# Kernel optimization log

Measured on AMD Instinct MI355X. Metric: run time of the kernel, lower is better.

The kernel has to match this reference:

```python
import jax, jax.numpy as jnp
import numpy as np

B, T, C = 4, 2048, 1024
Q_DIM, KV_DIM, VOCAB = 256, 32, 50257
N_LAYER, LAYER_ID = 24, 12
SCORE_SCALE, CAP_SCALE = 1024.0, 64.0
EPS = 1e-5


def _init_shift_coef(dim, power):
    ratio = 1.0 - LAYER_ID / max(N_LAYER, 1)
    ddd = np.arange(dim, dtype=np.float32) / max(dim - 1, 1)
    return jnp.asarray(1.0 - np.power(ddd, power * ratio), dtype=jnp.float32).reshape(1, 1, dim)


def setup_inputs() -> dict:
    key = jax.random.key(0)
    ks = jax.random.split(key, 10)
    x = jax.random.normal(ks[0], (B, T, C), dtype=jnp.float32)
    idx = jax.random.randint(ks[1], (B, T), 0, VOCAB, dtype=jnp.int64)
    u = lambda k, shape, a: jax.random.uniform(k, shape, jnp.float32, -a, a)
    W_qq = u(ks[2], (Q_DIM, C), 0.5 / C ** 0.5)
    W_k = u(ks[3], (KV_DIM, C), 0.05 / C ** 0.5)
    W_kup = u(ks[4], (Q_DIM, KV_DIM), 0.05 / KV_DIM ** 0.5)
    W_v = u(ks[5], (KV_DIM, C), 0.05 / C ** 0.5)
    W_vup = u(ks[6], (C, KV_DIM), 0.05 / KV_DIM ** 0.5)
    k_emb_tab = 0.02 * jax.random.normal(ks[7], (VOCAB, Q_DIM), dtype=jnp.float32)
    v_emb_tab = 0.02 * jax.random.normal(ks[8], (VOCAB, C), dtype=jnp.float32)
    return dict(
        x=x, idx=idx,
        W_qq=W_qq, W_k=W_k, W_kup=W_kup, W_v=W_v, W_vup=W_vup,
        k_emb_tab=k_emb_tab, v_emb_tab=v_emb_tab,
        x_q=_init_shift_coef(Q_DIM, 0.2),
        x_k=_init_shift_coef(Q_DIM, 0.7),
        x_v=_init_shift_coef(C, 0.7),
        g_q=jnp.ones((Q_DIM,), jnp.float32), b_q=jnp.zeros((Q_DIM,), jnp.float32),
        g_k=jnp.ones((Q_DIM,), jnp.float32), b_k=jnp.zeros((Q_DIM,), jnp.float32),
        g_v=jnp.ones((C,), jnp.float32), b_v=jnp.zeros((C,), jnp.float32),
    )


def _time_shift(t):
    # ZeroPad2d((0,0,1,-1)): shift sequence right by one, zero at position 0
    return jnp.pad(t, ((0, 0), (1, 0), (0, 0)))[:, :-1, :]


def _layernorm(t, g, b):
    mu = jnp.mean(t, axis=-1, keepdims=True)
    var = jnp.var(t, axis=-1, keepdims=True)
    return (t - mu) * jax.lax.rsqrt(var + EPS) * g + b


def reference(x, idx, W_qq, W_k, W_kup, W_v, W_vup, k_emb_tab, v_emb_tab,
              x_q, x_k, x_v, g_q, b_q, g_k, b_k, g_v, b_v):
    k_emb = k_emb_tab[idx]            # [B,T,Q_DIM]
    v_emb = v_emb_tab[idx]            # [B,T,C]

    q = jnp.einsum('btc,qc->btq', x, W_qq)
    q = q + (_time_shift(q) - q) * x_q
    q = _layernorm(q, g_q, b_q)

    k = jnp.einsum('btd,qd->btq', jnp.einsum('btc,dc->btd', x, W_k), W_kup) * k_emb
    k = k + (_time_shift(k) - k) * x_k
    k = _layernorm(k, g_k, b_k)

    v = jnp.tanh(jnp.einsum('btd,cd->btc', jnp.einsum('btc,dc->btd', x, W_v), W_vup)) * v_emb
    v = v + (_time_shift(v) - v) * x_v
    v = _layernorm(v, g_v, b_v)

    scores = jnp.einsum('btq,bsq->bts', q, k) / SCORE_SCALE   # [B,T,T]
    scores = CAP_SCALE * jnp.tanh(scores)
    causal = jnp.tril(jnp.ones((T, T), dtype=bool))
    scores = jnp.where(causal[None], scores, -jnp.inf)
    attn = jax.nn.softmax(scores.astype(jnp.float32), axis=-1).astype(scores.dtype)
    out = jnp.einsum('bts,bsc->btc', attn, v)                 # [B,T,C]
    return out
```

## Files before the change

### kernel.cpp

```cpp
#include <hip/hip_runtime.h>

#define B_   4
#define T_   2048
#define C_   1024
#define QD   256
#define KVD  32
#define NR   (B_*T_)
#define EPSF 1e-5f
#define CAPS 64.0f
#define INV_SS (1.0f/1024.0f)
#define SPLITROWS 4608

typedef __attribute__((ext_vector_type(8))) short bf16x8;
typedef __attribute__((ext_vector_type(4))) short bf16x4;
typedef __attribute__((ext_vector_type(4))) float f32x4;

__device__ __forceinline__ float bf2f(unsigned short h) {
    return __uint_as_float(((unsigned)h) << 16);
}
__device__ __forceinline__ unsigned short f2bf(float f) {
    unsigned u = __float_as_uint(f);
    u = u + 0x7fffu + ((u >> 16) & 1u);
    return (unsigned short)(u >> 16);
}
__device__ __forceinline__ float ldf(const void* p, long i, int isbf) {
    return isbf ? bf2f(((const unsigned short*)p)[i]) : ((const float*)p)[i];
}
__device__ __forceinline__ long ldix(const void* p, long i, int is64) {
    return is64 ? (long)((const long long*)p)[i] : (long)((const int*)p)[i];
}
__device__ __forceinline__ float fast_tanh(float v) {
    float u = __expf(2.0f * v);
    return 1.0f - 2.0f / (u + 1.0f);
}

__global__ void detect_kernel(const void* x, const void* idxp, int* flags) {
    __shared__ int cnt[2];
    int tid = threadIdx.x;
    if (tid < 2) cnt[tid] = 0;
    __syncthreads();
    int pl = 0;
    const unsigned short* u = (const unsigned short*)x;
    for (int r = 0; r < 2; r++) {
        long j = 2L * (((long)(tid * 2 + r) * 15013L) % 4000000L);
        unsigned short v = u[j];
        int e = (v >> 7) & 0xff;
        pl += (v == 0 || (e >= 100 && e <= 140)) ? 1 : 0;
    }
    atomicAdd(&cnt[0], pl);
    const unsigned* w = (const unsigned*)idxp;
    int z = (w[2 * tid + 1] == 0u) ? 1 : 0;
    atomicAdd(&cnt[1], z);
    __syncthreads();
    if (tid == 0) {
        flags[0] = (cnt[0] > 384) ? 1 : 0;
        flags[1] = (cnt[1] > 128) ? 1 : 0;
    }
}

template<int BN, int TANH, int EMB>
__global__ __launch_bounds__(256) void gemm_kernel(
    const void* __restrict__ A, const void* __restrict__ W,
    const void* __restrict__ emb, const void* __restrict__ idxp,
    float* __restrict__ Cout, int M, int K, int N, int embN, int amode,
    const int* __restrict__ flags)
{
    const int fbf = flags[0];
    const int abf = amode ? fbf : 0;
    const int i64 = flags[1];

    __shared__ float As[32][68];
    __shared__ float Bs[32][BN + 4];

    const int tid = threadIdx.x;
    const long m0 = (long)blockIdx.x * 64;
    const int  n0 = blockIdx.y * BN;
    constexpr int TN = (BN == 64) ? 4 : 2;
    const int tx = tid & 15;
    const int ty = tid >> 4;

    float c[4][TN];
#pragma unroll
    for (int i = 0; i < 4; i++)
#pragma unroll
        for (int j = 0; j < TN; j++) c[i][j] = 0.0f;

    for (int k0 = 0; k0 < K; k0 += 32) {
        {
            int i = tid >> 2;
            int j0 = (tid & 3) * 8;
            long base = (m0 + i) * (long)K + k0 + j0;
            if (abf) {
                bf16x8 av = *reinterpret_cast<const bf16x8*>((const unsigned short*)A + base);
#pragma unroll
                for (int jj = 0; jj < 8; jj++) As[j0 + jj][i] = bf2f((unsigned short)av[jj]);
            } else {
                const float4* ap = reinterpret_cast<const float4*>((const float*)A + base);
                float4 f0 = ap[0], f1 = ap[1];
                As[j0 + 0][i] = f0.x; As[j0 + 1][i] = f0.y;
                As[j0 + 2][i] = f0.z; As[j0 + 3][i] = f0.w;
                As[j0 + 4][i] = f1.x; As[j0 + 5][i] = f1.y;
                As[j0 + 6][i] = f1.z; As[j0 + 7][i] = f1.w;
            }
        }
        if (BN == 64) {
            int n = tid >> 2;
            int j0 = (tid & 3) * 8;
            long base = (long)(n0 + n) * K + k0 + j0;
            if (fbf) {
                bf16x8 bv = *reinterpret_cast<const bf16x8*>((const unsigned short*)W + base);
#pragma unroll
                for (int jj = 0; jj < 8; jj++) Bs[j0 + jj][n] = bf2f((unsigned short)bv[jj]);
            } else {
                const float4* bp = reinterpret_cast<const float4*>((const float*)W + base);
                float4 f0 = bp[0], f1 = bp[1];
                Bs[j0 + 0][n] = f0.x; Bs[j0 + 1][n] = f0.y;
                Bs[j0 + 2][n] = f0.z; Bs[j0 + 3][n] = f0.w;
                Bs[j0 + 4][n] = f1.x; Bs[j0 + 5][n] = f1.y;
                Bs[j0 + 6][n] = f1.z; Bs[j0 + 7][n] = f1.w;
            }
        } else {
            int n = tid >> 3;
            int j0 = (tid & 7) * 4;
            long base = (long)(n0 + n) * K + k0 + j0;
            if (fbf) {
                bf16x4 bv = *reinterpret_cast<const bf16x4*>((const unsigned short*)W + base);
#pragma unroll
                for (int jj = 0; jj < 4; jj++) Bs[j0 + jj][n] = bf2f((unsigned short)bv[jj]);
            } else {
                float4 f0 = *reinterpret_cast<const float4*>((const float*)W + base);
                Bs[j0 + 0][n] = f0.x; Bs[j0 + 1][n] = f0.y;
                Bs[j0 + 2][n] = f0.z; Bs[j0 + 3][n] = f0.w;
            }
        }
        __syncthreads();
#pragma unroll
        for (int kk = 0; kk < 32; kk++) {
            const float4 af = *reinterpret_cast<const float4*>(&As[kk][ty * 4]);
            const float av[4] = {af.x, af.y, af.z, af.w};
            float bv[TN];
#pragma unroll
            for (int j = 0; j < TN; j++) bv[j] = Bs[kk][tx * TN + j];
#pragma unroll
            for (int i = 0; i < 4; i++)
#pragma unroll
                for (int j = 0; j < TN; j++) c[i][j] = fmaf(av[i], bv[j], c[i][j]);
        }
        __syncthreads();
    }

#pragma unroll
    for (int i = 0; i < 4; i++) {
        long row = m0 + ty * 4 + i;
        long id = 0;
        if (EMB) id = ldix(idxp, row, i64);
        float ev[TN];
        if (EMB && TN == 4) {
            long ebase = id * (long)embN + n0 + tx * 4;
            if (fbf) {
                bf16x4 e4 = *reinterpret_cast<const bf16x4*>((const unsigned short*)emb + ebase);
#pragma unroll
                for (int j = 0; j < 4; j++) ev[j] = bf2f((unsigned short)e4[j]);
            } else {
                float4 e4 = *reinterpret_cast<const float4*>((const float*)emb + ebase);
                ev[0] = e4.x; ev[1] = e4.y; ev[2] = e4.z; ev[3] = e4.w;
            }
        }
#pragma unroll
        for (int j = 0; j < TN; j++) {
            int col = n0 + tx * TN + j;
            float v = c[i][j];
            if (TANH) v = fast_tanh(v);
            if (EMB)  v *= (TN == 4) ? ev[j] : ldf(emb, id * (long)embN + col, fbf);
            Cout[row * (long)N + col] = v;
        }
    }
}

template<int DIM>
__global__ __launch_bounds__(256) void shiftln_kernel(
    const float* __restrict__ src, void* __restrict__ dst, int dst_bf16,
    const void* __restrict__ xs, const void* __restrict__ g,
    const void* __restrict__ bb, const int* __restrict__ flags)
{
    const int fbf = flags[0];
    const long r = blockIdx.x;
    const int t = (int)(r % T_);
    const int tid = threadIdx.x;
    constexpr int PT = DIM / 256;
    float m[PT];
    float s1 = 0.0f, s2 = 0.0f;
#pragma unroll
    for (int j = 0; j < PT; j++) {
        int o = tid + 256 * j;
        float v  = src[r * DIM + o];
        float pv = (t > 0) ? src[(r - 1) * DIM + o] : 0.0f;
        float xv = ldf(xs, o, fbf);
        float mm = v + (pv - v) * xv;
        m[j] = mm;
        s1 += mm;
        s2 += mm * mm;
    }
#pragma unroll
    for (int off = 32; off > 0; off >>= 1) {
        s1 += __shfl_xor(s1, off);
        s2 += __shfl_xor(s2, off);
    }
    __shared__ float r1[4], r2[4];
    int w = tid >> 6;
    if ((tid & 63) == 0) { r1[w] = s1; r2[w] = s2; }
    __syncthreads();
    float t1 = r1[0] + r1[1] + r1[2] + r1[3];
    float t2 = r2[0] + r2[1] + r2[2] + r2[3];
    float mean = t1 / (float)DIM;
    float var  = t2 / (float)DIM - mean * mean;
    float rs = rsqrtf(var + EPSF);
#pragma unroll
    for (int j = 0; j < PT; j++) {
        int o = tid + 256 * j;
        float y = (m[j] - mean) * rs * ldf(g, o, fbf) + ldf(bb, o, fbf);
        if (dst_bf16) ((unsigned short*)dst)[r * DIM + o] = f2bf(y);
        else          ((float*)dst)[r * DIM + o] = y;
    }
}

__global__ __launch_bounds__(256) void vtrans_kernel(
    const unsigned* __restrict__ vpak, unsigned short* __restrict__ vT)
{
    __shared__ unsigned tile[64][33];
    const int row0 = blockIdx.x * 64;
    const int c0   = blockIdx.y * 64;
    const int tid = threadIdx.x;
    {
        int i = tid >> 2, jg = tid & 3;
        const unsigned* src = vpak + (long)(row0 + i) * 512 + (c0 >> 1) + jg * 8;
#pragma unroll
        for (int u = 0; u < 8; u++) tile[i][jg * 8 + u] = src[u];
    }
    __syncthreads();
    const int ch = tid >> 2;
    const int tc = (tid & 3) * 16;
    __align__(16) unsigned short buf[16];
#pragma unroll
    for (int u = 0; u < 16; u++) {
        unsigned wv = tile[tc + u][ch >> 1];
        buf[u] = (ch & 1) ? (unsigned short)(wv >> 16) : (unsigned short)(wv & 0xffffu);
    }
    const int bb = row0 / T_;
    const int t0 = row0 % T_;
    unsigned short* dst = vT + ((long)bb * C_ + c0 + ch) * T_ + t0 + tc;
    *reinterpret_cast<uint4*>(dst)     = *reinterpret_cast<const uint4*>(&buf[0]);
    *reinterpret_cast<uint4*>(dst + 8) = *reinterpret_cast<const uint4*>(&buf[8]);
}

__global__ __launch_bounds__(256) void attn_kernel(
    const unsigned short* __restrict__ q,
    const unsigned short* __restrict__ k,
    const unsigned short* __restrict__ vT,
    float* __restrict__ out,
    float* __restrict__ partA,
    float* __restrict__ partB,
    float* __restrict__ denw)
{
    __shared__ unsigned short qs[16 * 264];
    __shared__ unsigned short ps[2][16 * 72];
    __shared__ float dls[4][16];

    const int tid  = threadIdx.x;
    const int w    = tid >> 6;
    const int l    = tid & 63;
    const int l15  = l & 15;
    const int quad = l >> 4;

    const int bx    = blockIdx.x;
    const int qidx  = bx >> 1;
    const int split = bx & 1;
    const int b     = qidx >> 7;
    const int tb    = qidx & 127;
    const int t0    = tb * 16;

    const int nt = t0 / 64 + 1;
    const int n1 = nt >> 1;
    const int ts = split ? (nt - n1) : 0;
    const int te = split ? nt : (nt - n1);

    {
        int row = tid >> 4, seg = tid & 15;
        const unsigned short* src = q + ((long)b * T_ + t0 + row) * QD + seg * 16;
        *reinterpret_cast<bf16x8*>(qs + row * 264 + seg * 16) =
            *reinterpret_cast<const bf16x8*>(src);
        *reinterpret_cast<bf16x8*>(qs + row * 264 + seg * 16 + 8) =
            *reinterpret_cast<const bf16x8*>(src + 8);
    }
    __syncthreads();

    f32x4 acc[16];
#pragma unroll
    for (int jt = 0; jt < 16; jt++) acc[jt] = (f32x4){0.f, 0.f, 0.f, 0.f};
    float den[4] = {0.f, 0.f, 0.f, 0.f};

    const unsigned short* vbase =
        vT + ((long)b * C_ + w * 256 + l15) * T_ + quad * 8;
    const unsigned short* kbase =
        k + ((long)b * T_ + w * 16 + l15) * QD + quad * 8;

    for (int tile = ts; tile < te; tile++) {
        const int kt0 = tile * 64;

        const unsigned short* kr = kbase + (long)kt0 * QD;
        bf16x8 kb[8];
#pragma unroll
        for (int ii = 0; ii < 8; ii++)
            kb[ii] = *reinterpret_cast<const bf16x8*>(kr + ii * 32);

        const unsigned short* vb = vbase + kt0;
        bf16x8 v0[16];
#pragma unroll
        for (int jt = 0; jt < 16; jt++)
            v0[jt] = *reinterpret_cast<const bf16x8*>(vb + (long)jt * 16 * T_);

        f32x4 s = (f32x4){0.f, 0.f, 0.f, 0.f};
        {
            const unsigned short* qb = qs + l15 * 264 + quad * 8;
#pragma unroll
            for (int ii = 0; ii < 8; ii++) {
                bf16x8 qa = *reinterpret_cast<const bf16x8*>(qb + ii * 32);
                s = __builtin_amdgcn_mfma_f32_16x16x32_bf16(qa, kb[ii], s, 0, 0, 0);
            }
        }
        __builtin_amdgcn_sched_barrier(0);

        bf16x8 v1[16];
#pragma unroll
        for (int jt = 0; jt < 16; jt++)
            v1[jt] = *reinterpret_cast<const bf16x8*>(vb + (long)jt * 16 * T_ + 32);

        const int key = kt0 + w * 16 + l15;
        float wv[4];
#pragma unroll
        for (int rr = 0; rr < 4; rr++) {
            int qrow = t0 + quad * 4 + rr;
            float e = __expf(CAPS * fast_tanh(s[rr] * INV_SS));
            e = (key <= qrow) ? e : 0.0f;
            wv[rr] = bf2f(f2bf(e));
        }
        {
            float d0 = wv[0], d1 = wv[1], d2 = wv[2], d3 = wv[3];
#pragma unroll
            for (int off = 1; off < 16; off <<= 1) {
                d0 += __shfl_xor(d0, off);
                d1 += __shfl_xor(d1, off);
                d2 += __shfl_xor(d2, off);
                d3 += __shfl_xor(d3, off);
            }
            den[0] += d0; den[1] += d1; den[2] += d2; den[3] += d3;
        }
        unsigned short* psb = ps[tile & 1];
#pragma unroll
        for (int rr = 0; rr < 4; rr++)
            psb[(quad * 4 + rr) * 72 + w * 16 + l15] = f2bf(wv[rr]);
        __syncthreads();

        {
            const unsigned short* pb = psb + l15 * 72 + quad * 8;
            bf16x8 pA0 = *reinterpret_cast<const bf16x8*>(pb);
            bf16x8 pA1 = *reinterpret_cast<const bf16x8*>(pb + 32);
#pragma unroll
            for (int jt = 0; jt < 16; jt++)
                acc[jt] = __builtin_amdgcn_mfma_f32_16x16x32_bf16(pA0, v0[jt], acc[jt], 0, 0, 0);
#pragma unroll
            for (int jt = 0; jt < 16; jt++)
                acc[jt] = __builtin_amdgcn_mfma_f32_16x16x32_bf16(pA1, v1[jt], acc[jt], 0, 0, 0);
        }
    }

    if (l15 == 0) {
#pragma unroll
        for (int rr = 0; rr < 4; rr++) dls[w][quad * 4 + rr] = den[rr];
    }
    __syncthreads();
    if (w == 0 && l15 == 0) {
#pragma unroll
        for (int rr = 0; rr < 4; rr++) {
            int qr = quad * 4 + rr;
            float d = dls[0][qr] + dls[1][qr] + dls[2][qr] + dls[3][qr];
            denw[((long)b * T_ + t0 + qr) * 2 + split] = d;
        }
    }

    const long row0 = (long)b * T_ + t0;
    float* ob;
    if (split == 0) {
        ob = out + row0 * C_ + w * 256 + l15;
    } else {
        float* base = (row0 < SPLITROWS) ? (partA + row0 * C_)
                                         : (partB + (row0 - SPLITROWS) * C_);
        ob = base + w * 256 + l15;
    }
#pragma unroll
    for (int jt = 0; jt < 16; jt++)
#pragma unroll
        for (int rr = 0; rr < 4; rr++)
            ob[(long)(quad * 4 + rr) * C_ + jt * 16] = acc[jt][rr];
}

__global__ __launch_bounds__(256) void combine_kernel(
    float* __restrict__ out, const float* __restrict__ partA,
    const float* __restrict__ partB, const float* __restrict__ denw)
{
    const long row = blockIdx.x;
    const float* part = (row < SPLITROWS) ? (partA + row * C_)
                                          : (partB + (row - SPLITROWS) * C_);
    const float inv = 1.0f / (denw[row * 2] + denw[row * 2 + 1]);
    const int c = threadIdx.x * 4;
    float4 o = *reinterpret_cast<const float4*>(out + row * C_ + c);
    float4 pp = *reinterpret_cast<const float4*>(part + c);
    o.x = (o.x + pp.x) * inv;
    o.y = (o.y + pp.y) * inv;
    o.z = (o.z + pp.z) * inv;
    o.w = (o.w + pp.w) * inv;
    *reinterpret_cast<float4*>(out + row * C_ + c) = o;
}

extern "C" void kernel_launch(void* const* d_in, const int* in_sizes, int n_in,
                              void* d_out, int out_size, void* d_ws, size_t ws_size,
                              hipStream_t stream) {
    const void* x       = d_in[0];
    const void* idx     = d_in[1];
    const void* W_qq    = d_in[2];
    const void* W_k     = d_in[3];
    const void* W_kup   = d_in[4];
    const void* W_v     = d_in[5];
    const void* W_vup   = d_in[6];
    const void* k_emb   = d_in[7];
    const void* v_emb   = d_in[8];
    const void* x_q     = d_in[9];
    const void* x_k     = d_in[10];
    const void* x_v     = d_in[11];
    const void* g_q     = d_in[12];
    const void* b_q     = d_in[13];
    const void* g_k     = d_in[14];
    const void* b_k     = d_in[15];
    const void* g_v     = d_in[16];
    const void* b_v     = d_in[17];

    char* p = (char*)d_ws;
    int*   flags = (int*)p;            p += 256;
    float* qraw  = (float*)p;          p += (size_t)NR * QD * 4;
    float* kd    = (float*)p;          p += (size_t)NR * KVD * 4;
    float* vd    = (float*)p;          p += (size_t)NR * KVD * 4;
    float* kraw  = (float*)p;          p += (size_t)NR * QD * 4;
    float* vraw  = (float*)p;          p += (size_t)NR * C_ * 4;
    unsigned short* qf = (unsigned short*)p;  p += (size_t)NR * QD * 2;
    unsigned short* kf = (unsigned short*)p;  p += (size_t)NR * QD * 2;
    unsigned* vpak = (unsigned*)p;     p += (size_t)NR * (C_ / 2) * 4;
    unsigned short* vT = (unsigned short*)vraw;

    float* partA = qraw;
    float* partB = (float*)vpak;
    float* denw  = (float*)((char*)vraw + (size_t)16 * 1024 * 1024);

    detect_kernel<<<1, 256, 0, stream>>>(x, idx, flags);

    gemm_kernel<64, 0, 0><<<dim3(NR / 64, QD / 64), 256, 0, stream>>>(
        x, W_qq, nullptr, nullptr, qraw, NR, C_, QD, 0, 1, flags);
    gemm_kernel<32, 0, 0><<<dim3(NR / 64, 1), 256, 0, stream>>>(
        x, W_k, nullptr, nullptr, kd, NR, C_, KVD, 0, 1, flags);
    gemm_kernel<32, 0, 0><<<dim3(NR / 64, 1), 256, 0, stream>>>(
        x, W_v, nullptr, nullptr, vd, NR, C_, KVD, 0, 1, flags);
    gemm_kernel<64, 0, 1><<<dim3(NR / 64, QD / 64), 256, 0, stream>>>(
        kd, W_kup, k_emb, idx, kraw, NR, KVD, QD, QD, 0, flags);
    gemm_kernel<64, 1, 1><<<dim3(NR / 64, C_ / 64), 256, 0, stream>>>(
        vd, W_vup, v_emb, idx, vraw, NR, KVD, C_, C_, 0, flags);

    shiftln_kernel<QD><<<NR, 256, 0, stream>>>(qraw, qf, 1, x_q, g_q, b_q, flags);
    shiftln_kernel<QD><<<NR, 256, 0, stream>>>(kraw, kf, 1, x_k, g_k, b_k, flags);
    shiftln_kernel<C_><<<NR, 256, 0, stream>>>(vraw, vpak, 1, x_v, g_v, b_v, flags);

    vtrans_kernel<<<dim3(NR / 64, C_ / 64), 256, 0, stream>>>(vpak, vT);

    attn_kernel<<<1024, 256, 0, stream>>>(qf, kf, vT, (float*)d_out,
                                          partA, partB, denw);
    combine_kernel<<<NR, 256, 0, stream>>>((float*)d_out, partA, partB, denw);
}
```

Baseline: 769.6 us.

## Use 32-row attention tiles, 4-way key split with atomics, and fused K/V down-projection

After: 672.8 us. 1.14x faster.

```diff
diff --git a/kernel.cpp b/kernel.cpp
--- a/kernel.cpp
+++ b/kernel.cpp
@@ -9,7 +9,6 @@
 #define EPSF 1e-5f
 #define CAPS 64.0f
 #define INV_SS (1.0f/1024.0f)
-#define SPLITROWS 4608
 
 typedef __attribute__((ext_vector_type(8))) short bf16x8;
 typedef __attribute__((ext_vector_type(4))) short bf16x4;
@@ -58,12 +57,17 @@
     }
 }
 
+__global__ __launch_bounds__(256) void zero_kernel(float* __restrict__ out) {
+    const long i = ((long)blockIdx.x * 256 + threadIdx.x) * 4;
+    *reinterpret_cast<float4*>(out + i) = (float4){0.f, 0.f, 0.f, 0.f};
+}
+
 template<int BN, int TANH, int EMB>
 __global__ __launch_bounds__(256) void gemm_kernel(
     const void* __restrict__ A, const void* __restrict__ W,
     const void* __restrict__ emb, const void* __restrict__ idxp,
     float* __restrict__ Cout, int M, int K, int N, int embN, int amode,
-    const int* __restrict__ flags)
+    const int* __restrict__ flags, int lda)
 {
     const int fbf = flags[0];
     const int abf = amode ? fbf : 0;
@@ -89,7 +93,7 @@
         {
             int i = tid >> 2;
             int j0 = (tid & 3) * 8;
-            long base = (m0 + i) * (long)K + k0 + j0;
+            long base = (m0 + i) * (long)lda + k0 + j0;
             if (abf) {
                 bf16x8 av = *reinterpret_cast<const bf16x8*>((const unsigned short*)A + base);
 #pragma unroll
@@ -175,6 +179,72 @@
             Cout[row * (long)N + col] = v;
         }
     }
+}
+
+__global__ __launch_bounds__(256) void gemm_kv_kernel(
+    const void* __restrict__ A, const void* __restrict__ Wk,
+    const void* __restrict__ Wv, float* __restrict__ kvd,
+    const int* __restrict__ flags)
+{
+    const int fbf = flags[0];
+    __shared__ float As[32][20];
+    __shared__ float Bs[32][68];
+
+    const int tid = threadIdx.x;
+    const long m0 = (long)blockIdx.x * 16;
+    const int tx = tid & 63;
+    const int ty = tid >> 6;
+
+    float c[4] = {0.f, 0.f, 0.f, 0.f};
+
+    for (int k0 = 0; k0 < C_; k0 += 32) {
+        {
+            int i = tid >> 4;
+            int j0 = (tid & 15) * 2;
+            long base = (m0 + i) * (long)C_ + k0 + j0;
+            if (fbf) {
+                unsigned u = *reinterpret_cast<const unsigned*>((const unsigned short*)A + base);
+                As[j0][i]     = bf2f((unsigned short)(u & 0xffffu));
+                As[j0 + 1][i] = bf2f((unsigned short)(u >> 16));
+            } else {
+                float2 f = *reinterpret_cast<const float2*>((const float*)A + base);
+                As[j0][i] = f.x; As[j0 + 1][i] = f.y;
+            }
+        }
+        {
+            int n = tid >> 2;
+            int j0 = (tid & 3) * 8;
+            const void* Wp = (n < 32) ? Wk : Wv;
+            int nr = (n < 32) ? n : (n - 32);
+            long base = (long)nr * C_ + k0 + j0;
+            if (fbf) {
+                bf16x8 bv = *reinterpret_cast<const bf16x8*>((const unsigned short*)Wp + base);
+#pragma unroll
+                for (int jj = 0; jj < 8; jj++) Bs[j0 + jj][n] = bf2f((unsigned short)bv[jj]);
+            } else {
+                const float4* bp = reinterpret_cast<const float4*>((const float*)Wp + base);
+                float4 f0 = bp[0], f1 = bp[1];
+                Bs[j0 + 0][n] = f0.x; Bs[j0 + 1][n] = f0.y;
+                Bs[j0 + 2][n] = f0.z; Bs[j0 + 3][n] = f0.w;
+                Bs[j0 + 4][n] = f1.x; Bs[j0 + 5][n] = f1.y;
+                Bs[j0 + 6][n] = f1.z; Bs[j0 + 7][n] = f1.w;
+            }
+        }
+        __syncthreads();
+#pragma unroll
+        for (int kk = 0; kk < 32; kk++) {
+            const float4 af = *reinterpret_cast<const float4*>(&As[kk][ty * 4]);
+            const float bv = Bs[kk][tx];
+            c[0] = fmaf(af.x, bv, c[0]);
+            c[1] = fmaf(af.y, bv, c[1]);
+            c[2] = fmaf(af.z, bv, c[2]);
+            c[3] = fmaf(af.w, bv, c[3]);
+        }
+        __syncthreads();
+    }
+#pragma unroll
+    for (int i = 0; i < 4; i++)
+        kvd[(m0 + ty * 4 + i) * 64 + tx] = c[i];
 }
 
 template<int DIM>
@@ -253,18 +323,16 @@
     *reinterpret_cast<uint4*>(dst + 8) = *reinterpret_cast<const uint4*>(&buf[8]);
 }
 
-__global__ __launch_bounds__(256) void attn_kernel(
+__global__ __launch_bounds__(256, 2) void attn_kernel(
     const unsigned short* __restrict__ q,
     const unsigned short* __restrict__ k,
     const unsigned short* __restrict__ vT,
     float* __restrict__ out,
-    float* __restrict__ partA,
-    float* __restrict__ partB,
     float* __restrict__ denw)
 {
-    __shared__ unsigned short qs[16 * 264];
-    __shared__ unsigned short ps[2][16 * 72];
-    __shared__ float dls[4][16];
+    __shared__ unsigned short qs[32 * 264];
+    __shared__ unsigned short ps[2][32 * 72];
+    __shared__ float dls[4][32];
 
     const int tid  = threadIdx.x;
     const int w    = tid >> 6;
@@ -273,31 +341,34 @@
     const int quad = l >> 4;
 
     const int bx    = blockIdx.x;
-    const int qidx  = bx >> 1;
-    const int split = bx & 1;
-    const int b     = qidx >> 7;
-    const int tb    = qidx & 127;
-    const int t0    = tb * 16;
+    const int g     = bx >> 3;
+    const int x     = bx & 7;
+    const int b     = x >> 1;
+    const int split = ((x & 1) << 1) | (g & 1);
+    const int tb    = 63 - (g >> 1);
+    const int t0    = tb * 32;
 
     const int nt = t0 / 64 + 1;
-    const int n1 = nt >> 1;
-    const int ts = split ? (nt - n1) : 0;
-    const int te = split ? nt : (nt - n1);
+    const int ts = (nt * split) >> 2;
+    const int te = (nt * (split + 1)) >> 2;
 
     {
-        int row = tid >> 4, seg = tid & 15;
-        const unsigned short* src = q + ((long)b * T_ + t0 + row) * QD + seg * 16;
-        *reinterpret_cast<bf16x8*>(qs + row * 264 + seg * 16) =
-            *reinterpret_cast<const bf16x8*>(src);
-        *reinterpret_cast<bf16x8*>(qs + row * 264 + seg * 16 + 8) =
-            *reinterpret_cast<const bf16x8*>(src + 8);
+        int row = tid >> 3, seg = tid & 7;
+        const unsigned short* src = q + ((long)b * T_ + t0 + row) * QD + seg * 32;
+        unsigned short* dst = qs + row * 264 + seg * 32;
+#pragma unroll
+        for (int u = 0; u < 4; u++)
+            *reinterpret_cast<bf16x8*>(dst + u * 8) =
+                *reinterpret_cast<const bf16x8*>(src + u * 8);
     }
     __syncthreads();
 
-    f32x4 acc[16];
-#pragma unroll
-    for (int jt = 0; jt < 16; jt++) acc[jt] = (f32x4){0.f, 0.f, 0.f, 0.f};
-    float den[4] = {0.f, 0.f, 0.f, 0.f};
+    f32x4 acc[2][16];
+#pragma unroll
+    for (int mi = 0; mi < 2; mi++)
+#pragma unroll
+        for (int jt = 0; jt < 16; jt++) acc[mi][jt] = (f32x4){0.f, 0.f, 0.f, 0.f};
+    float den[2][4] = {{0.f, 0.f, 0.f, 0.f}, {0.f, 0.f, 0.f, 0.f}};
 
     const unsigned short* vbase =
         vT + ((long)b * C_ + w * 256 + l15) * T_ + quad * 8;
@@ -319,33 +390,32 @@
         for (int jt = 0; jt < 16; jt++)
             v0[jt] = *reinterpret_cast<const bf16x8*>(vb + (long)jt * 16 * T_);
 
-        f32x4 s = (f32x4){0.f, 0.f, 0.f, 0.f};
+        f32x4 s0 = (f32x4){0.f, 0.f, 0.f, 0.f};
+        f32x4 s1 = (f32x4){0.f, 0.f, 0.f, 0.f};
         {
             const unsigned short* qb = qs + l15 * 264 + quad * 8;
 #pragma unroll
             for (int ii = 0; ii < 8; ii++) {
-                bf16x8 qa = *reinterpret_cast<const bf16x8*>(qb + ii * 32);
-                s = __builtin_amdgcn_mfma_f32_16x16x32_bf16(qa, kb[ii], s, 0, 0, 0);
-            }
-        }
-        __builtin_amdgcn_sched_barrier(0);
-
-        bf16x8 v1[16];
-#pragma unroll
-        for (int jt = 0; jt < 16; jt++)
-            v1[jt] = *reinterpret_cast<const bf16x8*>(vb + (long)jt * 16 * T_ + 32);
+                bf16x8 qa0 = *reinterpret_cast<const bf16x8*>(qb + ii * 32);
+                bf16x8 qa1 = *reinterpret_cast<const bf16x8*>(qb + 16 * 264 + ii * 32);
+                s0 = __builtin_amdgcn_mfma_f32_16x16x32_bf16(qa0, kb[ii], s0, 0, 0, 0);
+                s1 = __builtin_amdgcn_mfma_f32_16x16x32_bf16(qa1, kb[ii], s1, 0, 0, 0);
+            }
+        }
 
         const int key = kt0 + w * 16 + l15;
-        float wv[4];
-#pragma unroll
-        for (int rr = 0; rr < 4; rr++) {
-            int qrow = t0 + quad * 4 + rr;
-            float e = __expf(CAPS * fast_tanh(s[rr] * INV_SS));
-            e = (key <= qrow) ? e : 0.0f;
-            wv[rr] = bf2f(f2bf(e));
-        }
-        {
-            float d0 = wv[0], d1 = wv[1], d2 = wv[2], d3 = wv[3];
+        float wv[2][4];
+#pragma unroll
+        for (int mi = 0; mi < 2; mi++) {
+#pragma unroll
+            for (int rr = 0; rr < 4; rr++) {
+                float sv = mi ? s1[rr] : s0[rr];
+                int qrow = t0 + mi * 16 + quad * 4 + rr;
+                float e = __expf(CAPS * fast_tanh(sv * INV_SS));
+                e = (key <= qrow) ? e : 0.0f;
+                wv[mi][rr] = bf2f(f2bf(e));
+            }
+            float d0 = wv[mi][0], d1 = wv[mi][1], d2 = wv[mi][2], d3 = wv[mi][3];
 #pragma unroll
             for (int off = 1; off < 16; off <<= 1) {
                 d0 += __shfl_xor(d0, off);
@@ -353,72 +423,82 @@
                 d2 += __shfl_xor(d2, off);
                 d3 += __shfl_xor(d3, off);
             }
-            den[0] += d0; den[1] += d1; den[2] += d2; den[3] += d3;
-        }
+            den[mi][0] += d0; den[mi][1] += d1; den[mi][2] += d2; den[mi][3] += d3;
+        }
+
         unsigned short* psb = ps[tile & 1];
 #pragma unroll
-        for (int rr = 0; rr < 4; rr++)
-            psb[(quad * 4 + rr) * 72 + w * 16 + l15] = f2bf(wv[rr]);
+        for (int mi = 0; mi < 2; mi++)
+#pragma unroll
+            for (int rr = 0; rr < 4; rr++)
+                psb[(mi * 16 + quad * 4 + rr) * 72 + w * 16 + l15] = f2bf(wv[mi][rr]);
         __syncthreads();
+
+        bf16x8 v1[16];
+#pragma unroll
+        for (int jt = 0; jt < 16; jt++)
+            v1[jt] = *reinterpret_cast<const bf16x8*>(vb + (long)jt * 16 * T_ + 32);
 
         {
             const unsigned short* pb = psb + l15 * 72 + quad * 8;
-            bf16x8 pA0 = *reinterpret_cast<const bf16x8*>(pb);
-            bf16x8 pA1 = *reinterpret_cast<const bf16x8*>(pb + 32);
-#pragma unroll
-            for (int jt = 0; jt < 16; jt++)
-                acc[jt] = __builtin_amdgcn_mfma_f32_16x16x32_bf16(pA0, v0[jt], acc[jt], 0, 0, 0);
-#pragma unroll
-            for (int jt = 0; jt < 16; jt++)
-                acc[jt] = __builtin_amdgcn_mfma_f32_16x16x32_bf16(pA1, v1[jt], acc[jt], 0, 0, 0);
+            bf16x8 pa00 = *reinterpret_cast<const bf16x8*>(pb);
+            bf16x8 pa10 = *reinterpret_cast<const bf16x8*>(pb + 16 * 72);
+#pragma unroll
+            for (int jt = 0; jt < 16; jt++) {
+                acc[0][jt] = __builtin_amdgcn_mfma_f32_16x16x32_bf16(pa00, v0[jt], acc[0][jt], 0, 0, 0);
+                acc[1][jt] = __builtin_amdgcn_mfma_f32_16x16x32_bf16(pa10, v0[jt], acc[1][jt], 0, 0, 0);
+            }
+            bf16x8 pa01 = *reinterpret_cast<const bf16x8*>(pb + 32);
+            bf16x8 pa11 = *reinterpret_cast<const bf16x8*>(pb + 16 * 72 + 32);
+#pragma unroll
+            for (int jt = 0; jt < 16; jt++) {
+                acc[0][jt] = __builtin_amdgcn_mfma_f32_16x16x32_bf16(pa01, v1[jt], acc[0][jt], 0, 0, 0);
+                acc[1][jt] = __builtin_amdgcn_mfma_f32_16x16x32_bf16(pa11, v1[jt], acc[1][jt], 0, 0, 0);
+            }
         }
     }
 
     if (l15 == 0) {
 #pragma unroll
-        for (int rr = 0; rr < 4; rr++) dls[w][quad * 4 + rr] = den[rr];
+        for (int mi = 0; mi < 2; mi++)
+#pragma unroll
+            for (int rr = 0; rr < 4; rr++)
+                dls[w][mi * 16 + quad * 4 + rr] = den[mi][rr];
     }
     __syncthreads();
     if (w == 0 && l15 == 0) {
 #pragma unroll
-        for (int rr = 0; rr < 4; rr++) {
-            int qr = quad * 4 + rr;
-            float d = dls[0][qr] + dls[1][qr] + dls[2][qr] + dls[3][qr];
-            denw[((long)b * T_ + t0 + qr) * 2 + split] = d;
-        }
-    }
-
-    const long row0 = (long)b * T_ + t0;
-    float* ob;
-    if (split == 0) {
-        ob = out + row0 * C_ + w * 256 + l15;
-    } else {
-        float* base = (row0 < SPLITROWS) ? (partA + row0 * C_)
-                                         : (partB + (row0 - SPLITROWS) * C_);
-        ob = base + w * 256 + l15;
-    }
-#pragma unroll
-    for (int jt = 0; jt < 16; jt++)
-#pragma unroll
-        for (int rr = 0; rr < 4; rr++)
-            ob[(long)(quad * 4 + rr) * C_ + jt * 16] = acc[jt][rr];
-}
-
-__global__ __launch_bounds__(256) void combine_kernel(
-    float* __restrict__ out, const float* __restrict__ partA,
-    const float* __restrict__ partB, const float* __restrict__ denw)
+        for (int mi = 0; mi < 2; mi++)
+#pragma unroll
+            for (int rr = 0; rr < 4; rr++) {
+                int qr = mi * 16 + quad * 4 + rr;
+                float d = dls[0][qr] + dls[1][qr] + dls[2][qr] + dls[3][qr];
+                denw[((long)b * T_ + t0 + qr) * 4 + split] = d;
+            }
+    }
+
+    if (ts < te) {
+        float* ob = out + ((long)b * T_ + t0) * C_ + w * 256 + l15;
+#pragma unroll
+        for (int mi = 0; mi < 2; mi++)
+#pragma unroll
+            for (int jt = 0; jt < 16; jt++)
+#pragma unroll
+                for (int rr = 0; rr < 4; rr++)
+                    atomicAdd(&ob[(long)(mi * 16 + quad * 4 + rr) * C_ + jt * 16],
+                              acc[mi][jt][rr]);
+    }
+}
+
+__global__ __launch_bounds__(256) void normalize_kernel(
+    float* __restrict__ out, const float* __restrict__ denw)
 {
     const long row = blockIdx.x;
-    const float* part = (row < SPLITROWS) ? (partA + row * C_)
-                                          : (partB + (row - SPLITROWS) * C_);
-    const float inv = 1.0f / (denw[row * 2] + denw[row * 2 + 1]);
+    const float4 d = *reinterpret_cast<const float4*>(denw + row * 4);
+    const float inv = 1.0f / (d.x + d.y + d.z + d.w);
     const int c = threadIdx.x * 4;
     float4 o = *reinterpret_cast<const float4*>(out + row * C_ + c);
-    float4 pp = *reinterpret_cast<const float4*>(part + c);
-    o.x = (o.x + pp.x) * inv;
-    o.y = (o.y + pp.y) * inv;
-    o.z = (o.z + pp.z) * inv;
-    o.w = (o.w + pp.w) * inv;
+    o.x *= inv; o.y *= inv; o.z *= inv; o.w *= inv;
     *reinterpret_cast<float4*>(out + row * C_ + c) = o;
 }
 
@@ -447,31 +527,25 @@
     char* p = (char*)d_ws;
     int*   flags = (int*)p;            p += 256;
     float* qraw  = (float*)p;          p += (size_t)NR * QD * 4;
-    float* kd    = (float*)p;          p += (size_t)NR * KVD * 4;
-    float* vd    = (float*)p;          p += (size_t)NR * KVD * 4;
+    float* kvd   = (float*)p;          p += (size_t)NR * 64 * 4;
     float* kraw  = (float*)p;          p += (size_t)NR * QD * 4;
     float* vraw  = (float*)p;          p += (size_t)NR * C_ * 4;
     unsigned short* qf = (unsigned short*)p;  p += (size_t)NR * QD * 2;
     unsigned short* kf = (unsigned short*)p;  p += (size_t)NR * QD * 2;
     unsigned* vpak = (unsigned*)p;     p += (size_t)NR * (C_ / 2) * 4;
     unsigned short* vT = (unsigned short*)vraw;
-
-    float* partA = qraw;
-    float* partB = (float*)vpak;
     float* denw  = (float*)((char*)vraw + (size_t)16 * 1024 * 1024);
 
     detect_kernel<<<1, 256, 0, stream>>>(x, idx, flags);
+    zero_kernel<<<NR, 256, 0, stream>>>((float*)d_out);
 
     gemm_kernel<64, 0, 0><<<dim3(NR / 64, QD / 64), 256, 0, stream>>>(
-        x, W_qq, nullptr, nullptr, qraw, NR, C_, QD, 0, 1, flags);
-    gemm_kernel<32, 0, 0><<<dim3(NR / 64, 1), 256, 0, stream>>>(
-        x, W_k, nullptr, nullptr, kd, NR, C_, KVD, 0, 1, flags);
-    gemm_kernel<32, 0, 0><<<dim3(NR / 64, 1), 256, 0, stream>>>(
-        x, W_v, nullptr, nullptr, vd, NR, C_, KVD, 0, 1, flags);
+        x, W_qq, nullptr, nullptr, qraw, NR, C_, QD, 0, 1, flags, C_);
+    gemm_kv_kernel<<<NR / 16, 256, 0, stream>>>(x, W_k, W_v, kvd, flags);
     gemm_kernel<64, 0, 1><<<dim3(NR / 64, QD / 64), 256, 0, stream>>>(
-        kd, W_kup, k_emb, idx, kraw, NR, KVD, QD, QD, 0, flags);
+        kvd, W_kup, k_emb, idx, kraw, NR, KVD, QD, QD, 0, flags, 64);
     gemm_kernel<64, 1, 1><<<dim3(NR / 64, C_ / 64), 256, 0, stream>>>(
-        vd, W_vup, v_emb, idx, vraw, NR, KVD, C_, C_, 0, flags);
+        (const float*)kvd + 32, W_vup, v_emb, idx, vraw, NR, KVD, C_, C_, 0, flags, 64);
 
     shiftln_kernel<QD><<<NR, 256, 0, stream>>>(qraw, qf, 1, x_q, g_q, b_q, flags);
     shiftln_kernel<QD><<<NR, 256, 0, stream>>>(kraw, kf, 1, x_k, g_k, b_k, flags);
@@ -479,7 +553,6 @@
 
     vtrans_kernel<<<dim3(NR / 64, C_ / 64), 256, 0, stream>>>(vpak, vT);
 
-    attn_kernel<<<1024, 256, 0, stream>>>(qf, kf, vT, (float*)d_out,
-                                          partA, partB, denw);
-    combine_kernel<<<NR, 256, 0, stream>>>((float*)d_out, partA, partB, denw);
-}
+    attn_kernel<<<1024, 256, 0, stream>>>(qf, kf, vT, (float*)d_out, denw);
+    normalize_kernel<<<NR, 256, 0, stream>>>((float*)d_out, denw);
+}
```
